# Kernel tuning notes

Hardware: AMD Instinct MI355X
Metric: run time of the kernel (lower is better)

The kernel has to match this reference:

```python
import jax, jax.numpy as jnp
import numpy as np

NEG = -1e30  # stand-in for -inf that keeps gradients finite


def setup_inputs() -> dict:
    key = jax.random.key(0)
    k0, k1, k2 = jax.random.split(key, 3)
    B, S, W, K = 48, 128, 4, 256
    logits = jax.random.normal(k0, (B, S, W, K), dtype=jnp.float32)
    T = jax.random.normal(k1, (B, K, K), dtype=jnp.float32)
    hamming_cost = jax.random.uniform(k2, (B, S, W, K), dtype=jnp.float32)
    tag_mask = jnp.ones((B, K, K), dtype=jnp.float32)
    text_mask = jnp.ones((B, S), dtype=jnp.int32)
    return dict(logits=logits, T=T, hamming_cost=hamming_cost,
                tag_mask=tag_mask, text_mask=text_mask)


def reference(logits, T, hamming_cost, tag_mask, text_mask):
    # Semi-Markov CRF partition function (use_transition_layer == 'True').
    B, S, W, K = logits.shape
    lg = jnp.transpose(logits, (1, 2, 0, 3))        # (S, W, B, K)
    hc = jnp.transpose(hamming_cost, (1, 2, 0, 3))  # (S, W, B, K)
    # emission score for a span of width w+1 ending at j, labeled k
    emit_all = (lg + hc) * tag_mask[:, 0, :]        # (S, W, B, K)
    tranT = T * tag_mask                            # (B, K, Kprev)
    w_idx = jnp.arange(W)

    # buf[w] = alpha[j - w]; rows with j - w < 0 held at NEG (excluded)
    buf0 = jnp.full((W, B, K), NEG, dtype=jnp.float32).at[0].set(0.0)

    def step(buf, inp):
        emit_j, j = inp  # emit_j: (W, B, K)
        # transition applies only when the previous alpha is a real segment
        # boundary (w < j); the w == j row connects to the initial state.
        tran = jnp.where((w_idx < j)[:, None, None, None], tranT[None], 0.0)
        # scores[w, b, k, kp] = alpha[j-w, b, kp] + T'[b, k, kp] + emit[w, b, k]
        scores = buf[:, :, None, :] + tran + emit_j[:, :, :, None]
        alpha_j = jax.nn.logsumexp(scores, axis=(0, 3))  # (B, K)
        buf = jnp.concatenate([alpha_j[None], buf[:-1]], axis=0)
        return buf, alpha_j

    _, alphas = jax.lax.scan(step, buf0, (emit_all, jnp.arange(S)))
    full = jnp.concatenate([jnp.zeros((1, B, K), dtype=jnp.float32), alphas], axis=0)
    ls = jax.nn.logsumexp(full, axis=-1)            # (S+1, B)
    lengths = jnp.sum(text_mask, axis=1)            # (B,)
    partition = ls[lengths, jnp.arange(B)]          # (B,)
    return partition[None]                          # (1, B) as in torch code
```

## Files before the change

kernel.cpp:

```cpp
#include <hip/hip_runtime.h>
#include <type_traits>
#include <cstdint>

typedef __attribute__((ext_vector_type(2))) _Float16 half2;
typedef __attribute__((ext_vector_type(4))) float f32x4;
typedef __attribute__((ext_vector_type(16))) unsigned int u32x16;

constexpr int CB = 48, CS = 128, CW = 4, CK = 256;

__global__ __launch_bounds__(256, 1)
void crf_scan_kernel(const float* __restrict__ logits,
                     const float* __restrict__ T,
                     const float* __restrict__ ham,
                     const float* __restrict__ tag_mask,
                     const int* __restrict__ text_mask,
                     float* __restrict__ out) {
    const int b = blockIdx.x;
    const int tid = (int)threadIdx.x;
    const int wv = tid >> 6;
    const int lane = tid & 63;

    __shared__ float plds[2][4][4][64];
    __shared__ f32x4 redl[2];
    __shared__ int len_s;

    if (tid == 0) len_s = 0;
    __syncthreads();
    if (tid < CS) atomicAdd(&len_s, text_mask[b * CS + tid]);
    if (tid == 0) redl[1] = (f32x4){64.0f, 64.0f, 64.0f, 64.0f};

    const float tm0 = tag_mask[(size_t)b * CK * CK + tid];

    u32x16 et0{}, et1{}, et2{}, et3{}, et4{}, et5{}, et6{}, et7{};
    {
        const float* Tb = T + (size_t)b * CK * CK;
        const float* mb = tag_mask + (size_t)b * CK * CK;
#define INIT_G(g, LO, HI) { \
        const float* tp = Tb + (64 * g + lane) * CK + 64 * wv; \
        const float* mp = mb + (64 * g + lane) * CK + 64 * wv; \
        _Pragma("unroll") \
        for (int i = 0; i < 16; ++i) { \
            float a0 = __expf(tp[2 * i] * mp[2 * i]); \
            float a1 = __expf(tp[2 * i + 1] * mp[2 * i + 1]); \
            LO[i] = __builtin_bit_cast(unsigned int, __builtin_amdgcn_cvt_pkrtz(a0, a1)); \
            float b0 = __expf(tp[32 + 2 * i] * mp[32 + 2 * i]); \
            float b1 = __expf(tp[32 + 2 * i + 1] * mp[32 + 2 * i + 1]); \
            HI[i] = __builtin_bit_cast(unsigned int, __builtin_amdgcn_cvt_pkrtz(b0, b1)); \
        } }
        INIT_G(0, et0, et1)
        INIT_G(1, et2, et3)
        INIT_G(2, et4, et5)
        INIT_G(3, et6, et7)
#undef INIT_G
    }

    const float* lgb = logits + (size_t)b * CS * CW * CK;
    const float* hcb = ham    + (size_t)b * CS * CW * CK;

    float Mn = 0.0f, M1 = 0.0f, M2 = 0.0f, M3 = 0.0f;
    float y1 = 0.0f, y2 = 0.0f, y3 = 0.0f;
    float ls_prev = __logf(256.0f) - 2.0f;
    float out_r = __logf(256.0f);

    float em_cur[4];
#pragma unroll
    for (int w = 0; w < 4; ++w)
        em_cur[w] = (lgb[w * CK + tid] + hcb[w * CK + tid]) * tm0;

    uint32_t pk = 0x3c003c00u;

    __syncthreads();
    const int len = len_s;

    auto step = [&](int j, auto pc) {
        constexpr int P = pc.value;

        float ac[8] = {0, 0, 0, 0, 0, 0, 0, 0};
#pragma unroll
        for (int i = 0; i < 16; ++i) {
            uint32_t s0 = (uint32_t)__builtin_amdgcn_readlane((int)pk, 2 * i);
            uint32_t s1 = (uint32_t)__builtin_amdgcn_readlane((int)pk, 2 * i + 32);
            half2 h0 = __builtin_bit_cast(half2, s0);
            half2 h1 = __builtin_bit_cast(half2, s1);
            ac[0] = __builtin_amdgcn_fdot2(__builtin_bit_cast(half2, et0[i]), h0, ac[0], false);
            ac[4] = __builtin_amdgcn_fdot2(__builtin_bit_cast(half2, et1[i]), h1, ac[4], false);
            ac[1] = __builtin_amdgcn_fdot2(__builtin_bit_cast(half2, et2[i]), h0, ac[1], false);
            ac[5] = __builtin_amdgcn_fdot2(__builtin_bit_cast(half2, et3[i]), h1, ac[5], false);
            ac[2] = __builtin_amdgcn_fdot2(__builtin_bit_cast(half2, et4[i]), h0, ac[2], false);
            ac[6] = __builtin_amdgcn_fdot2(__builtin_bit_cast(half2, et5[i]), h1, ac[6], false);
            ac[3] = __builtin_amdgcn_fdot2(__builtin_bit_cast(half2, et6[i]), h0, ac[3], false);
            ac[7] = __builtin_amdgcn_fdot2(__builtin_bit_cast(half2, et7[i]), h1, ac[7], false);
        }

        int jn = (j + 1 < CS) ? j + 1 : 0;
        float lgn[4], hcn[4];
#pragma unroll
        for (int w = 0; w < 4; ++w) {
            int idx = jn * (CW * CK) + w * CK + tid;
            lgn[w] = lgb[idx];
            hcn[w] = hcb[idx];
        }

#pragma unroll
        for (int g = 0; g < 4; ++g)
            plds[P][wv][g][lane] = ac[g] + ac[g + 4];

        asm volatile("s_waitcnt expcnt(0) lgkmcnt(0)\n\ts_barrier" ::: "memory");

        float yn = plds[P][0][wv][lane] + plds[P][1][wv][lane] +
                   plds[P][2][wv][lane] + plds[P][3][wv][lane];

        f32x4 rv = redl[1 - P];
        float sum_prev = (rv[0] + rv[1]) + (rv[2] + rv[3]);
        float lsj = Mn + __logf(sum_prev);
        if (j == len) out_r = lsj;
        float delta = lsj - ls_prev;
        ls_prev = lsj;
        float Mj = lsj + delta;
        float C = Mn;

        float S;
        {   float yv = yn;
            if (j == 0) yv = 256.0f;
            S = yv * __expf(Mn + em_cur[0] - C);
        }
        {   float yv = y1;
            if (j < 4) yv = (j == 1) ? 256.0f : ((j < 1) ? 0.0f : yv);
            S = fmaf(yv, __expf(M1 + em_cur[1] - C), S);
        }
        {   float yv = y2;
            if (j < 4) yv = (j == 2) ? 256.0f : ((j < 2) ? 0.0f : yv);
            S = fmaf(yv, __expf(M2 + em_cur[2] - C), S);
        }
        {   float yv = y3;
            if (j < 4) yv = (j == 3) ? 256.0f : ((j < 3) ? 0.0f : yv);
            S = fmaf(yv, __expf(M3 + em_cur[3] - C), S);
        }
        float e = S * __expf(C - Mj);

        float partner = __shfl_xor(e, 1, 64);
        float lo = (lane & 1) ? partner : e;
        float hi = (lane & 1) ? e : partner;
        pk = __builtin_bit_cast(uint32_t, __builtin_amdgcn_cvt_pkrtz(lo, hi));
        float ps = e + partner;
#pragma unroll
        for (int o = 2; o < 64; o <<= 1) ps += __shfl_xor(ps, o, 64);
        if (lane == 0) ((float*)&redl[P])[wv] = ps;

        y3 = y2; y2 = y1; y1 = yn;
        M3 = M2; M2 = M1; M1 = Mn; Mn = Mj;
#pragma unroll
        for (int w = 0; w < 4; ++w)
            em_cur[w] = (lgn[w] + hcn[w]) * tm0;
    };

    for (int j = 0; j < CS; j += 2) {
        step(j,     std::integral_constant<int, 0>{});
        step(j + 1, std::integral_constant<int, 1>{});
    }

    __syncthreads();
    if (tid == 0) {
        f32x4 rv = redl[1];
        float tot = (rv[0] + rv[1]) + (rv[2] + rv[3]);
        float ls_full = Mn + __logf(tot);
        if (len == CS) out_r = ls_full;
        out[b] = out_r;
    }
}

extern "C" void kernel_launch(void* const* d_in, const int* in_sizes, int n_in,
                              void* d_out, int out_size, void* d_ws, size_t ws_size,
                              hipStream_t stream) {
    const float* logits    = (const float*)d_in[0];
    const float* T         = (const float*)d_in[1];
    const float* ham       = (const float*)d_in[2];
    const float* tag_mask  = (const float*)d_in[3];
    const int*   text_mask = (const int*)d_in[4];
    float* out = (float*)d_out;

    crf_scan_kernel<<<CB, 256, 0, stream>>>(logits, T, ham, tag_mask, text_mask, out);
}
```

Before: 203.6 us.

## Split matvec across 8 waves and broadcast alpha via LDS fp16 buffer

Doubles the block to 512 threads so each wave holds half as many packed transition registers and handles a 32-column slice of the K×K matvec. The previous-step alpha vector is shared through an fp16 LDS buffer instead of readlane broadcasts, and the normalizer is computed with an extra dot against ones rather than a per-step shuffle reduction. The trade-off is a second barrier per step, idle upper waves during the epilogue, and an 8-way partial-sum reduction through LDS.

```diff
diff --git a/kernel.cpp b/kernel.cpp
--- a/kernel.cpp
+++ b/kernel.cpp
@@ -4,11 +4,12 @@
 
 typedef __attribute__((ext_vector_type(2))) _Float16 half2;
 typedef __attribute__((ext_vector_type(4))) float f32x4;
+typedef __attribute__((ext_vector_type(4))) unsigned int u32x4;
 typedef __attribute__((ext_vector_type(16))) unsigned int u32x16;
 
 constexpr int CB = 48, CS = 128, CW = 4, CK = 256;
 
-__global__ __launch_bounds__(256, 1)
+__global__ __launch_bounds__(512, 2)
 void crf_scan_kernel(const float* __restrict__ logits,
                      const float* __restrict__ T,
                      const float* __restrict__ ham,
@@ -17,40 +18,37 @@
                      float* __restrict__ out) {
     const int b = blockIdx.x;
     const int tid = (int)threadIdx.x;
-    const int wv = tid >> 6;
+    const int w8 = tid >> 6;
     const int lane = tid & 63;
+    const bool epi = (tid < CK);
 
-    __shared__ float plds[2][4][4][64];
-    __shared__ f32x4 redl[2];
+    __shared__ alignas(16) unsigned short ebuf16[CK];
+    __shared__ float plds[4][8][64];
+    __shared__ alignas(16) float pldo[8];
+    __shared__ float red4[4];
     __shared__ int len_s;
 
     if (tid == 0) len_s = 0;
     __syncthreads();
     if (tid < CS) atomicAdd(&len_s, text_mask[b * CS + tid]);
-    if (tid == 0) redl[1] = (f32x4){64.0f, 64.0f, 64.0f, 64.0f};
+    if (tid < CK) ebuf16[tid] = 0x3C00;
 
-    const float tm0 = tag_mask[(size_t)b * CK * CK + tid];
+    const float tm0 = tag_mask[(size_t)b * CK * CK + (tid & (CK - 1))];
 
-    u32x16 et0{}, et1{}, et2{}, et3{}, et4{}, et5{}, et6{}, et7{};
+    u32x16 et0{}, et1{}, et2{}, et3{};
     {
         const float* Tb = T + (size_t)b * CK * CK;
         const float* mb = tag_mask + (size_t)b * CK * CK;
-#define INIT_G(g, LO, HI) { \
-        const float* tp = Tb + (64 * g + lane) * CK + 64 * wv; \
-        const float* mp = mb + (64 * g + lane) * CK + 64 * wv; \
+#define INIT_G(g, V) { \
+        const float* tp = Tb + (64 * g + lane) * CK + 32 * w8; \
+        const float* mp = mb + (64 * g + lane) * CK + 32 * w8; \
         _Pragma("unroll") \
         for (int i = 0; i < 16; ++i) { \
             float a0 = __expf(tp[2 * i] * mp[2 * i]); \
             float a1 = __expf(tp[2 * i + 1] * mp[2 * i + 1]); \
-            LO[i] = __builtin_bit_cast(unsigned int, __builtin_amdgcn_cvt_pkrtz(a0, a1)); \
-            float b0 = __expf(tp[32 + 2 * i] * mp[32 + 2 * i]); \
-            float b1 = __expf(tp[32 + 2 * i + 1] * mp[32 + 2 * i + 1]); \
-            HI[i] = __builtin_bit_cast(unsigned int, __builtin_amdgcn_cvt_pkrtz(b0, b1)); \
+            V[i] = __builtin_bit_cast(unsigned int, __builtin_amdgcn_cvt_pkrtz(a0, a1)); \
         } }
-        INIT_G(0, et0, et1)
-        INIT_G(1, et2, et3)
-        INIT_G(2, et4, et5)
-        INIT_G(3, et6, et7)
+        INIT_G(0, et0) INIT_G(1, et1) INIT_G(2, et2) INIT_G(3, et3)
 #undef INIT_G
     }
 
@@ -61,108 +59,116 @@
     float y1 = 0.0f, y2 = 0.0f, y3 = 0.0f;
     float ls_prev = __logf(256.0f) - 2.0f;
     float out_r = __logf(256.0f);
+    float e_last = 0.0f;
 
     float em_cur[4];
+    if (epi) {
 #pragma unroll
-    for (int w = 0; w < 4; ++w)
-        em_cur[w] = (lgb[w * CK + tid] + hcb[w * CK + tid]) * tm0;
-
-    uint32_t pk = 0x3c003c00u;
+        for (int w = 0; w < 4; ++w)
+            em_cur[w] = (lgb[w * CK + tid] + hcb[w * CK + tid]) * tm0;
+    }
 
     __syncthreads();
     const int len = len_s;
+    const half2 ones = {(_Float16)1.0f, (_Float16)1.0f};
 
-    auto step = [&](int j, auto pc) {
-        constexpr int P = pc.value;
-
-        float ac[8] = {0, 0, 0, 0, 0, 0, 0, 0};
-#pragma unroll
-        for (int i = 0; i < 16; ++i) {
-            uint32_t s0 = (uint32_t)__builtin_amdgcn_readlane((int)pk, 2 * i);
-            uint32_t s1 = (uint32_t)__builtin_amdgcn_readlane((int)pk, 2 * i + 32);
-            half2 h0 = __builtin_bit_cast(half2, s0);
-            half2 h1 = __builtin_bit_cast(half2, s1);
-            ac[0] = __builtin_amdgcn_fdot2(__builtin_bit_cast(half2, et0[i]), h0, ac[0], false);
-            ac[4] = __builtin_amdgcn_fdot2(__builtin_bit_cast(half2, et1[i]), h1, ac[4], false);
-            ac[1] = __builtin_amdgcn_fdot2(__builtin_bit_cast(half2, et2[i]), h0, ac[1], false);
-            ac[5] = __builtin_amdgcn_fdot2(__builtin_bit_cast(half2, et3[i]), h1, ac[5], false);
-            ac[2] = __builtin_amdgcn_fdot2(__builtin_bit_cast(half2, et4[i]), h0, ac[2], false);
-            ac[6] = __builtin_amdgcn_fdot2(__builtin_bit_cast(half2, et5[i]), h1, ac[6], false);
-            ac[3] = __builtin_amdgcn_fdot2(__builtin_bit_cast(half2, et6[i]), h0, ac[3], false);
-            ac[7] = __builtin_amdgcn_fdot2(__builtin_bit_cast(half2, et7[i]), h1, ac[7], false);
-        }
+    for (int j = 0; j < CS; ++j) {
+        u32x4 evq0 = *(const u32x4*)(&ebuf16[32 * w8]);
+        u32x4 evq1 = *(const u32x4*)(&ebuf16[32 * w8 + 8]);
+        u32x4 evq2 = *(const u32x4*)(&ebuf16[32 * w8 + 16]);
+        u32x4 evq3 = *(const u32x4*)(&ebuf16[32 * w8 + 24]);
 
         int jn = (j + 1 < CS) ? j + 1 : 0;
         float lgn[4], hcn[4];
+        if (epi) {
 #pragma unroll
-        for (int w = 0; w < 4; ++w) {
-            int idx = jn * (CW * CK) + w * CK + tid;
-            lgn[w] = lgb[idx];
-            hcn[w] = hcb[idx];
+            for (int w = 0; w < 4; ++w) {
+                int idx = jn * (CW * CK) + w * CK + tid;
+                lgn[w] = lgb[idx];
+                hcn[w] = hcb[idx];
+            }
         }
 
-#pragma unroll
-        for (int g = 0; g < 4; ++g)
-            plds[P][wv][g][lane] = ac[g] + ac[g + 4];
+        float ac0 = 0.0f, ac1 = 0.0f, ac2 = 0.0f, ac3 = 0.0f, aco = 0.0f;
+#define DOT4(EVQ, base) \
+        _Pragma("unroll") \
+        for (int i = 0; i < 4; ++i) { \
+            half2 h = __builtin_bit_cast(half2, EVQ[i]); \
+            ac0 = __builtin_amdgcn_fdot2(__builtin_bit_cast(half2, et0[base + i]), h, ac0, false); \
+            ac1 = __builtin_amdgcn_fdot2(__builtin_bit_cast(half2, et1[base + i]), h, ac1, false); \
+            ac2 = __builtin_amdgcn_fdot2(__builtin_bit_cast(half2, et2[base + i]), h, ac2, false); \
+            ac3 = __builtin_amdgcn_fdot2(__builtin_bit_cast(half2, et3[base + i]), h, ac3, false); \
+            aco = __builtin_amdgcn_fdot2(ones, h, aco, false); \
+        }
+        DOT4(evq0, 0) DOT4(evq1, 4) DOT4(evq2, 8) DOT4(evq3, 12)
+#undef DOT4
+
+        plds[0][w8][lane] = ac0;
+        plds[1][w8][lane] = ac1;
+        plds[2][w8][lane] = ac2;
+        plds[3][w8][lane] = ac3;
+        if (lane == 0) pldo[w8] = aco;
 
         asm volatile("s_waitcnt expcnt(0) lgkmcnt(0)\n\ts_barrier" ::: "memory");
 
-        float yn = plds[P][0][wv][lane] + plds[P][1][wv][lane] +
-                   plds[P][2][wv][lane] + plds[P][3][wv][lane];
+        if (epi) {
+            const int g = tid >> 6;
+            float yn = ((plds[g][0][lane] + plds[g][1][lane]) +
+                        (plds[g][2][lane] + plds[g][3][lane])) +
+                       ((plds[g][4][lane] + plds[g][5][lane]) +
+                        (plds[g][6][lane] + plds[g][7][lane]));
+            f32x4 po0 = *(const f32x4*)(&pldo[0]);
+            f32x4 po1 = *(const f32x4*)(&pldo[4]);
+            float sum_prev = ((po0[0] + po0[1]) + (po0[2] + po0[3])) +
+                             ((po1[0] + po1[1]) + (po1[2] + po1[3]));
 
-        f32x4 rv = redl[1 - P];
-        float sum_prev = (rv[0] + rv[1]) + (rv[2] + rv[3]);
-        float lsj = Mn + __logf(sum_prev);
-        if (j == len) out_r = lsj;
-        float delta = lsj - ls_prev;
-        ls_prev = lsj;
-        float Mj = lsj + delta;
-        float C = Mn;
+            float lsj = Mn + __logf(sum_prev);
+            if (j == len) out_r = lsj;
+            float delta = lsj - ls_prev;
+            ls_prev = lsj;
+            float Mj = lsj + delta;
+            float C = Mn;
 
-        float S;
-        {   float yv = yn;
-            if (j == 0) yv = 256.0f;
-            S = yv * __expf(Mn + em_cur[0] - C);
+            float S;
+            {   float yv = yn;
+                if (j == 0) yv = 256.0f;
+                S = yv * __expf(Mn + em_cur[0] - C);
+            }
+            {   float yv = y1;
+                if (j < 4) yv = (j == 1) ? 256.0f : ((j < 1) ? 0.0f : yv);
+                S = fmaf(yv, __expf(M1 + em_cur[1] - C), S);
+            }
+            {   float yv = y2;
+                if (j < 4) yv = (j == 2) ? 256.0f : ((j < 2) ? 0.0f : yv);
+                S = fmaf(yv, __expf(M2 + em_cur[2] - C), S);
+            }
+            {   float yv = y3;
+                if (j < 4) yv = (j == 3) ? 256.0f : ((j < 3) ? 0.0f : yv);
+                S = fmaf(yv, __expf(M3 + em_cur[3] - C), S);
+            }
+            float e = S * __expf(C - Mj);
+            ebuf16[tid] = __builtin_bit_cast(unsigned short, (_Float16)e);
+            e_last = e;
+
+            y3 = y2; y2 = y1; y1 = yn;
+            M3 = M2; M2 = M1; M1 = Mn; Mn = Mj;
+#pragma unroll
+            for (int w = 0; w < 4; ++w)
+                em_cur[w] = (lgn[w] + hcn[w]) * tm0;
         }
-        {   float yv = y1;
-            if (j < 4) yv = (j == 1) ? 256.0f : ((j < 1) ? 0.0f : yv);
-            S = fmaf(yv, __expf(M1 + em_cur[1] - C), S);
-        }
-        {   float yv = y2;
-            if (j < 4) yv = (j == 2) ? 256.0f : ((j < 2) ? 0.0f : yv);
-            S = fmaf(yv, __expf(M2 + em_cur[2] - C), S);
-        }
-        {   float yv = y3;
-            if (j < 4) yv = (j == 3) ? 256.0f : ((j < 3) ? 0.0f : yv);
-            S = fmaf(yv, __expf(M3 + em_cur[3] - C), S);
-        }
-        float e = S * __expf(C - Mj);
 
-        float partner = __shfl_xor(e, 1, 64);
-        float lo = (lane & 1) ? partner : e;
-        float hi = (lane & 1) ? e : partner;
-        pk = __builtin_bit_cast(uint32_t, __builtin_amdgcn_cvt_pkrtz(lo, hi));
-        float ps = e + partner;
-#pragma unroll
-        for (int o = 2; o < 64; o <<= 1) ps += __shfl_xor(ps, o, 64);
-        if (lane == 0) ((float*)&redl[P])[wv] = ps;
-
-        y3 = y2; y2 = y1; y1 = yn;
-        M3 = M2; M2 = M1; M1 = Mn; Mn = Mj;
-#pragma unroll
-        for (int w = 0; w < 4; ++w)
-            em_cur[w] = (lgn[w] + hcn[w]) * tm0;
-    };
-
-    for (int j = 0; j < CS; j += 2) {
-        step(j,     std::integral_constant<int, 0>{});
-        step(j + 1, std::integral_constant<int, 1>{});
+        asm volatile("s_waitcnt expcnt(0) lgkmcnt(0)\n\ts_barrier" ::: "memory");
     }
 
+    if (epi) {
+        float ps = e_last;
+#pragma unroll
+        for (int o = 1; o < 64; o <<= 1) ps += __shfl_xor(ps, o, 64);
+        if (lane == 0) red4[tid >> 6] = ps;
+    }
     __syncthreads();
     if (tid == 0) {
-        f32x4 rv = redl[1];
-        float tot = (rv[0] + rv[1]) + (rv[2] + rv[3]);
+        float tot = (red4[0] + red4[1]) + (red4[2] + red4[3]);
         float ls_full = Mn + __logf(tot);
         if (len == CS) out_r = ls_full;
         out[b] = out_r;
@@ -179,5 +185,5 @@
     const int*   text_mask = (const int*)d_in[4];
     float* out = (float*)d_out;
 
-    crf_scan_kernel<<<CB, 256, 0, stream>>>(logits, T, ham, tag_mask, text_mask, out);
+    crf_scan_kernel<<<CB, 512, 0, stream>>>(logits, T, ham, tag_mask, text_mask, out);
 }
```

New measurement: 203.5 us. Within noise of the previous version (-0.0%).
